# Optimization experiments

Measured on AMD Instinct MI355X. Metric: run time of the kernel, lower is better.

Reference implementation:

```python
import jax, jax.numpy as jnp
import numpy as np

B, S, I, H, A = 512, 256, 12, 256, 9


def _lstm_layer(x, w_ih, w_hh, b_ih, b_hh):
    # x: [B,S,in] -> outputs [B,S,H], final (h, c). PyTorch gate order i,f,g,o.
    b, s, _ = x.shape
    h_dim = w_hh.shape[1]
    xg = jnp.einsum('bsi,gi->bsg', x, w_ih) + b_ih  # [B,S,4H] precomputed input gates

    def step(carry, xg_t):
        h, c = carry
        gates = xg_t + h @ w_hh.T + b_hh
        i_g, f_g, g_g, o_g = jnp.split(gates, 4, axis=-1)
        c = jax.nn.sigmoid(f_g) * c + jax.nn.sigmoid(i_g) * jnp.tanh(g_g)
        h = jax.nn.sigmoid(o_g) * jnp.tanh(c)
        return (h, c), h

    init = (jnp.zeros((b, h_dim), x.dtype), jnp.zeros((b, h_dim), x.dtype))
    (h, c), ys = jax.lax.scan(step, init, jnp.swapaxes(xg, 0, 1))
    return jnp.swapaxes(ys, 0, 1), h, c


def setup_inputs() -> dict:
    key = jax.random.key(0)
    ks = jax.random.split(key, 20)
    sc = 0.1
    inp = {
        'x': jax.random.normal(ks[0], (B, S, I), jnp.float32),
        'mask': jnp.ones((B, A), jnp.float32),
        'W_emb': jax.random.normal(ks[1], (H, I), jnp.float32) * sc,
        'b_emb': jnp.zeros((H,), jnp.float32),
        'w_ih0': jax.random.normal(ks[2], (4 * H, H), jnp.float32) * sc,
        'w_hh0': jax.random.normal(ks[3], (4 * H, H), jnp.float32) * sc,
        'b_ih0': jnp.zeros((4 * H,), jnp.float32),
        'b_hh0': jnp.zeros((4 * H,), jnp.float32),
        'w_ih1': jax.random.normal(ks[4], (4 * H, H), jnp.float32) * sc,
        'w_hh1': jax.random.normal(ks[5], (4 * H, H), jnp.float32) * sc,
        'b_ih1': jnp.zeros((4 * H,), jnp.float32),
        'b_hh1': jnp.zeros((4 * H,), jnp.float32),
        'ln_g': jnp.ones((H,), jnp.float32),
        'ln_b': jnp.zeros((H,), jnp.float32),
        'w1': jax.random.normal(ks[6], (32, H), jnp.float32) * sc,
        'b1': jnp.zeros((32,), jnp.float32),
        'w2': jax.random.normal(ks[7], (A, 32), jnp.float32) * sc,
        'b2': jnp.zeros((A,), jnp.float32),
    }
    return inp


def reference(x, mask, W_emb, b_emb, w_ih0, w_hh0, b_ih0, b_hh0,
              w_ih1, w_hh1, b_ih1, b_hh1, ln_g, ln_b, w1, b1, w2, b2):
    # embed + ReLU
    emb = jax.nn.relu(jnp.einsum('bsi,hi->bsh', x, W_emb) + b_emb)  # [B,S,H]
    # 2-layer LSTM (dropout between layers is identity in eval mode)
    y0, h0, c0 = _lstm_layer(emb, w_ih0, w_hh0, b_ih0, b_hh0)
    y1, h1, c1 = _lstm_layer(y0, w_ih1, w_hh1, b_ih1, b_hh1)
    last = y1[:, -1, :]  # [B,H]
    # LayerNorm
    mu = jnp.mean(last, axis=-1, keepdims=True)
    var = jnp.mean((last - mu) ** 2, axis=-1, keepdims=True)
    normed = (last - mu) / jnp.sqrt(var + 1e-5) * ln_g + ln_b
    # MLP head (dropout identity in eval)
    hdn = jax.nn.relu(normed @ w1.T + b1)
    logits = hdn @ w2.T + b2  # [B,A]
    logits = logits + (1.0 - mask) * -1e9
    hidden = (jnp.stack([h0, h1]), jnp.stack([c0, c1]))
    return logits, hidden
```

## Files before the change

kernel.cpp:

```cpp
#include <hip/hip_runtime.h>
#include <cstdint>
#include <cstddef>

typedef __attribute__((ext_vector_type(8))) short short8;
typedef __attribute__((ext_vector_type(4))) float f32x4;

#define MFMA16(a, b, c) __builtin_amdgcn_mfma_f32_16x16x32_bf16((a), (b), (c), 0, 0, 0)

constexpr int kB = 512, kS = 256, kI = 12, kH = 256, kA = 9;
constexpr int kNS = 8;
constexpr int kNB = 32;
constexpr int kT  = 512;
constexpr int LDH = 264;
constexpr int LDG = 132;
constexpr int kBH = kB * kH;
constexpr int FLS = kS * kNS;

constexpr int OUT_H = kB * kA;
constexpr int OUT_C = OUT_H + 2 * kBH;

__device__ __forceinline__ short f2bf(float f) {
  uint32_t u = __float_as_uint(f);
  u += 0x7fffu + ((u >> 16) & 1u);
  return (short)(u >> 16);
}
__device__ __forceinline__ float fast_sigmoid(float v) {
  return __builtin_amdgcn_rcpf(1.f + __expf(-v));
}
__device__ __forceinline__ float fast_tanh(float v) {
  return 2.f * __builtin_amdgcn_rcpf(1.f + __expf(-2.f * v)) - 1.f;
}

__global__ __launch_bounds__(kT) void lstm_scan_kernel(
    const float* __restrict__ x,
    const float* __restrict__ W_emb, const float* __restrict__ b_emb,
    const float* __restrict__ w_ih0, const float* __restrict__ w_hh0,
    const float* __restrict__ b_ih0, const float* __restrict__ b_hh0,
    const float* __restrict__ w_ih1, const float* __restrict__ w_hh1,
    const float* __restrict__ b_ih1, const float* __restrict__ b_hh1,
    unsigned short* __restrict__ h0ex, unsigned short* __restrict__ h1ex,
    int* __restrict__ flags,
    float* __restrict__ dout)
{
  const int tid   = threadIdx.x;
  const int btile = blockIdx.x & (kNB - 1);
  const int slice = blockIdx.x >> 5;
  const int b0    = btile * 16;
  const int lane  = tid & 63;
  const int wave  = tid >> 6;
  const int n16   = lane & 15;
  const int quad  = lane >> 4;

  __shared__ short embL[2][16 * LDH];
  __shared__ short hA[16 * LDH];
  __shared__ short hB[16 * LDH];
  __shared__ float gL0[16 * LDG];
  __shared__ float gL1[16 * LDG];

  for (int i = tid; i < 16 * LDH; i += kT) { hA[i] = 0; hB[i] = 0; }

  const float* Wm[4] = { w_ih0, w_hh0, w_ih1, w_hh1 };
  short8 wB[4][8];
  {
    const int gcol = (wave >> 1) * kH + slice * 32 + (wave & 1) * 16 + n16;
#pragma unroll
    for (int mat = 0; mat < 4; ++mat) {
      const float* wp = Wm[mat] + (size_t)gcol * kH;
#pragma unroll
      for (int kk = 0; kk < 8; ++kk) {
        const float* p = wp + kk * 32 + quad * 8;
        const float4 f0 = *(const float4*)p;
        const float4 f1 = *(const float4*)(p + 4);
        short8 v;
        v[0] = f2bf(f0.x); v[1] = f2bf(f0.y); v[2] = f2bf(f0.z); v[3] = f2bf(f0.w);
        v[4] = f2bf(f1.x); v[5] = f2bf(f1.y); v[6] = f2bf(f1.z); v[7] = f2bf(f1.w);
        wB[mat][kk] = v;
      }
    }
  }
  short8 wE[2];
  float bembv[2];
#pragma unroll
  for (int i = 0; i < 2; ++i) {
    const int col = wave * 32 + i * 16 + n16;
    short8 v;
#pragma unroll
    for (int j = 0; j < 8; ++j) {
      const int k = quad * 8 + j;
      v[j] = (k < kI) ? f2bf(W_emb[col * kI + k]) : (short)0;
    }
    wE[i] = v;
    bembv[i] = b_emb[col];
  }
  const int erow = tid >> 5;
  const int ec   = tid & 31;
  const int ecol = slice * 32 + ec;
  float bi0[4], bi1[4];
#pragma unroll
  for (int g = 0; g < 4; ++g) {
    bi0[g] = b_ih0[g * kH + ecol] + b_hh0[g * kH + ecol];
    bi1[g] = b_ih1[g * kH + ecol] + b_hh1[g * kH + ecol];
  }
  float c0v = 0.f, c1v = 0.f;

#define EMB_TILE(DST, T)                                                    \
  {                                                                         \
    const float* xr = x + ((size_t)(b0 + n16) * kS + (T)) * kI;             \
    short8 xa;                                                              \
    _Pragma("unroll")                                                       \
    for (int j = 0; j < 8; ++j) {                                           \
      const int k = quad * 8 + j;                                           \
      xa[j] = (k < kI) ? f2bf(xr[k]) : (short)0;                            \
    }                                                                       \
    _Pragma("unroll")                                                       \
    for (int i = 0; i < 2; ++i) {                                           \
      f32x4 zz = {0.f, 0.f, 0.f, 0.f};                                      \
      f32x4 e = MFMA16(xa, wE[i], zz);                                      \
      const int col = wave * 32 + i * 16 + n16;                             \
      _Pragma("unroll")                                                     \
      for (int r = 0; r < 4; ++r) {                                         \
        float v = e[r] + bembv[i];                                          \
        v = v > 0.f ? v : 0.f;                                              \
        (DST)[(quad * 4 + r) * LDH + col] = f2bf(v);                        \
      }                                                                     \
    }                                                                       \
  }

  EMB_TILE(embL[0], 0);
  EMB_TILE(embL[1], 1);
  __syncthreads();
  f32x4 zcur = {0.f, 0.f, 0.f, 0.f};
#pragma unroll
  for (int kk = 0; kk < 8; ++kk) {
    const short8 e = *(const short8*)&embL[0][n16 * LDH + kk * 32 + quad * 8];
    zcur = MFMA16(e, wB[0][kk], zcur);
  }

  int* const fl = flags + btile * FLS;

  for (int p = 0; p <= kS; ++p) {
    const int par = p & 1;

    {
      f32x4 a0 = zcur;
      f32x4 g1 = {0.f, 0.f, 0.f, 0.f};
#pragma unroll
      for (int kk = 0; kk < 8; ++kk) {
        const short8 ha = *(const short8*)&hA[n16 * LDH + kk * 32 + quad * 8];
        a0 = MFMA16(ha, wB[1][kk], a0);
        g1 = MFMA16(ha, wB[2][kk], g1);
      }
#pragma unroll
      for (int kk = 0; kk < 8; ++kk) {
        const short8 hb = *(const short8*)&hB[n16 * LDH + kk * 32 + quad * 8];
        g1 = MFMA16(hb, wB[3][kk], g1);
      }
      const int lcol = (wave >> 1) * 32 + (wave & 1) * 16 + n16;
#pragma unroll
      for (int r = 0; r < 4; ++r) {
        gL0[(quad * 4 + r) * LDG + lcol] = a0[r];
        gL1[(quad * 4 + r) * LDG + lcol] = g1[r];
      }
    }
    __syncthreads();

    if (p < kS) {
      const float iv = gL0[erow * LDG +       ec] + bi0[0];
      const float fv = gL0[erow * LDG +  32 + ec] + bi0[1];
      const float gv = gL0[erow * LDG +  64 + ec] + bi0[2];
      const float ov = gL0[erow * LDG +  96 + ec] + bi0[3];
      const float c = fast_sigmoid(fv) * c0v + fast_sigmoid(iv) * fast_tanh(gv);
      c0v = c;
      const float h = fast_sigmoid(ov) * fast_tanh(c);
      unsigned short* dst = &h0ex[(size_t)par * kBH + (size_t)(b0 + erow) * kH + ecol];
      __hip_atomic_store(dst, (unsigned short)f2bf(h), __ATOMIC_RELAXED, __HIP_MEMORY_SCOPE_AGENT);
      if (p == kS - 1) {
        dout[OUT_H + (size_t)(b0 + erow) * kH + ecol] = h;
        dout[OUT_C + (size_t)(b0 + erow) * kH + ecol] = c;
      }
    }
    if (p >= 1) {
      const float iv = gL1[erow * LDG +       ec] + bi1[0];
      const float fv = gL1[erow * LDG +  32 + ec] + bi1[1];
      const float gv = gL1[erow * LDG +  64 + ec] + bi1[2];
      const float ov = gL1[erow * LDG +  96 + ec] + bi1[3];
      const float c = fast_sigmoid(fv) * c1v + fast_sigmoid(iv) * fast_tanh(gv);
      c1v = c;
      const float h = fast_sigmoid(ov) * fast_tanh(c);
      unsigned short* dst = &h1ex[(size_t)par * kBH + (size_t)(b0 + erow) * kH + ecol];
      __hip_atomic_store(dst, (unsigned short)f2bf(h), __ATOMIC_RELAXED, __HIP_MEMORY_SCOPE_AGENT);
      if (p == kS) {
        dout[OUT_H + kBH + (size_t)(b0 + erow) * kH + ecol] = h;
        dout[OUT_C + kBH + (size_t)(b0 + erow) * kH + ecol] = c;
      }
    }
    __syncthreads();

    if (p < kS) {
      if (tid == 0)
        __hip_atomic_store(fl + p * kNS + slice, p + 1,
                           __ATOMIC_RELAXED, __HIP_MEMORY_SCOPE_AGENT);

      f32x4 z = {0.f, 0.f, 0.f, 0.f};
#pragma unroll
      for (int kk = 0; kk < 8; ++kk) {
        const short8 e = *(const short8*)&embL[par ^ 1][n16 * LDH + kk * 32 + quad * 8];
        z = MFMA16(e, wB[0][kk], z);
      }

      {
        const uint64_t* f64 = (const uint64_t*)(fl + p * kNS);
        const int tgt = p + 1;
        for (;;) {
          uint64_t v0 = __hip_atomic_load(f64 + 0, __ATOMIC_RELAXED, __HIP_MEMORY_SCOPE_AGENT);
          uint64_t v1 = __hip_atomic_load(f64 + 1, __ATOMIC_RELAXED, __HIP_MEMORY_SCOPE_AGENT);
          uint64_t v2 = __hip_atomic_load(f64 + 2, __ATOMIC_RELAXED, __HIP_MEMORY_SCOPE_AGENT);
          uint64_t v3 = __hip_atomic_load(f64 + 3, __ATOMIC_RELAXED, __HIP_MEMORY_SCOPE_AGENT);
          if ((int)(v0 & 0xffffffffu) >= tgt && (int)(v0 >> 32) >= tgt &&
              (int)(v1 & 0xffffffffu) >= tgt && (int)(v1 >> 32) >= tgt &&
              (int)(v2 & 0xffffffffu) >= tgt && (int)(v2 >> 32) >= tgt &&
              (int)(v3 & 0xffffffffu) >= tgt && (int)(v3 >> 32) >= tgt)
            break;
          __builtin_amdgcn_s_sleep(1);
        }
      }

      const int rr = tid >> 5;
      const int cc = (tid & 31) * 8;
      const size_t base = (size_t)par * kBH + (size_t)(b0 + rr) * kH + cc;
      const uint64_t* s0 = (const uint64_t*)&h0ex[base];
      const uint64_t* s1 = (const uint64_t*)&h1ex[base];
      uint64_t va0 = __hip_atomic_load(s0 + 0, __ATOMIC_RELAXED, __HIP_MEMORY_SCOPE_AGENT);
      uint64_t va1 = __hip_atomic_load(s0 + 1, __ATOMIC_RELAXED, __HIP_MEMORY_SCOPE_AGENT);
      uint64_t vb0 = __hip_atomic_load(s1 + 0, __ATOMIC_RELAXED, __HIP_MEMORY_SCOPE_AGENT);
      uint64_t vb1 = __hip_atomic_load(s1 + 1, __ATOMIC_RELAXED, __HIP_MEMORY_SCOPE_AGENT);

      if (p + 2 < kS) EMB_TILE(embL[par], p + 2);

      uint64_t* dA = (uint64_t*)&hA[rr * LDH + cc];
      uint64_t* dB = (uint64_t*)&hB[rr * LDH + cc];
      dA[0] = va0; dA[1] = va1;
      dB[0] = vb0; dB[1] = vb1;
      __syncthreads();
      zcur = z;
    }
  }
#undef EMB_TILE
}

__global__ __launch_bounds__(64) void head_kernel(
    const float* __restrict__ h1last, const float* __restrict__ mask,
    const float* __restrict__ ln_g, const float* __restrict__ ln_b,
    const float* __restrict__ w1, const float* __restrict__ b1,
    const float* __restrict__ w2, const float* __restrict__ b2,
    float* __restrict__ out)
{
  const int r = blockIdx.x;
  const int lane = threadIdx.x;
  __shared__ float ns[kH];
  __shared__ float hd[32];
  const float4 v = *(const float4*)&h1last[r * kH + lane * 4];
  float vv[4] = {v.x, v.y, v.z, v.w};
  float s = vv[0] + vv[1] + vv[2] + vv[3];
#pragma unroll
  for (int off = 32; off > 0; off >>= 1) s += __shfl_xor(s, off, 64);
  const float mean = s * (1.f / kH);
  float q = 0.f;
#pragma unroll
  for (int j = 0; j < 4; ++j) { const float d = vv[j] - mean; q += d * d; }
#pragma unroll
  for (int off = 32; off > 0; off >>= 1) q += __shfl_xor(q, off, 64);
  const float rstd = rsqrtf(q * (1.f / kH) + 1e-5f);
#pragma unroll
  for (int j = 0; j < 4; ++j) {
    const int c = lane * 4 + j;
    ns[c] = (vv[j] - mean) * rstd * ln_g[c] + ln_b[c];
  }
  __syncthreads();
  if (lane < 32) {
    float a = b1[lane];
    const float* wr = w1 + lane * kH;
    for (int k = 0; k < kH; ++k) a += ns[k] * wr[k];
    hd[lane] = a > 0.f ? a : 0.f;
  }
  __syncthreads();
  if (lane < kA) {
    float a = b2[lane];
    const float* wr = w2 + lane * 32;
#pragma unroll
    for (int k = 0; k < 32; ++k) a += hd[k] * wr[k];
    a += (1.f - mask[r * kA + lane]) * (-1e9f);
    out[r * kA + lane] = a;
  }
}

extern "C" void kernel_launch(void* const* d_in, const int* in_sizes, int n_in,
                              void* d_out, int out_size, void* d_ws, size_t ws_size,
                              hipStream_t stream)
{
  (void)in_sizes; (void)n_in; (void)out_size; (void)ws_size;
  const float* x     = (const float*)d_in[0];
  const float* mask  = (const float*)d_in[1];
  const float* W_emb = (const float*)d_in[2];
  const float* b_emb = (const float*)d_in[3];
  const float* w_ih0 = (const float*)d_in[4];
  const float* w_hh0 = (const float*)d_in[5];
  const float* b_ih0 = (const float*)d_in[6];
  const float* b_hh0 = (const float*)d_in[7];
  const float* w_ih1 = (const float*)d_in[8];
  const float* w_hh1 = (const float*)d_in[9];
  const float* b_ih1 = (const float*)d_in[10];
  const float* b_hh1 = (const float*)d_in[11];
  const float* ln_g  = (const float*)d_in[12];
  const float* ln_b  = (const float*)d_in[13];
  const float* w1    = (const float*)d_in[14];
  const float* b1    = (const float*)d_in[15];
  const float* w2    = (const float*)d_in[16];
  const float* b2    = (const float*)d_in[17];
  float* out = (float*)d_out;

  unsigned short* h0ex = (unsigned short*)d_ws;
  unsigned short* h1ex = h0ex + 2 * kBH;
  int* flags = (int*)(h1ex + 2 * kBH);
  const size_t flag_bytes = (size_t)kNB * FLS * sizeof(int);

  hipMemsetAsync(flags, 0, flag_bytes, stream);
  hipMemsetAsync(h1ex, 0, (size_t)kBH * sizeof(unsigned short), stream);

  lstm_scan_kernel<<<dim3(kNB * kNS), dim3(kT), 0, stream>>>(
      x, W_emb, b_emb, w_ih0, w_hh0, b_ih0, b_hh0, w_ih1, w_hh1, b_ih1, b_hh1,
      h0ex, h1ex, flags, out);

  head_kernel<<<dim3(kB), dim3(64), 0, stream>>>(
      out + OUT_H + kBH, mask, ln_g, ln_b, w1, b1, w2, b2, out);
}
```

Before: 1.018 ms.

## Split hidden columns across 16 slices with 256-thread blocks, two per CU

Each batch tile's hidden dimension is now split into 16 slices instead of 8, giving 512 blocks of 256 threads with launch bounds allowing two blocks per CU. The block-to-tile mapping is swizzled so the two halves interleave. Each block now handles 16 gate columns, so per-step work per block is halved, but every block waits on 16 flags instead of 8. The input-gate product for layer 0 is no longer precomputed ahead of time; it is computed inside the step alongside the recurrent product, and the embedding uses a single buffer filled one step ahead. This adds more cross-block synchronisation and puts the embedding work back on the critical path, in exchange for more parallelism per step.

```diff
diff --git a/kernel.cpp b/kernel.cpp
--- a/kernel.cpp
+++ b/kernel.cpp
@@ -8,11 +8,11 @@
 #define MFMA16(a, b, c) __builtin_amdgcn_mfma_f32_16x16x32_bf16((a), (b), (c), 0, 0, 0)
 
 constexpr int kB = 512, kS = 256, kI = 12, kH = 256, kA = 9;
-constexpr int kNS = 8;
+constexpr int kNS = 16;
 constexpr int kNB = 32;
-constexpr int kT  = 512;
+constexpr int kT  = 256;
 constexpr int LDH = 264;
-constexpr int LDG = 132;
+constexpr int LDG2 = 68;
 constexpr int kBH = kB * kH;
 constexpr int FLS = kS * kNS;
 
@@ -31,7 +31,7 @@
   return 2.f * __builtin_amdgcn_rcpf(1.f + __expf(-2.f * v)) - 1.f;
 }
 
-__global__ __launch_bounds__(kT) void lstm_scan_kernel(
+__global__ __launch_bounds__(kT, 2) void lstm_scan_kernel(
     const float* __restrict__ x,
     const float* __restrict__ W_emb, const float* __restrict__ b_emb,
     const float* __restrict__ w_ih0, const float* __restrict__ w_hh0,
@@ -42,27 +42,30 @@
     int* __restrict__ flags,
     float* __restrict__ dout)
 {
-  const int tid   = threadIdx.x;
-  const int btile = blockIdx.x & (kNB - 1);
-  const int slice = blockIdx.x >> 5;
+  const int tid  = threadIdx.x;
+  const int bid  = blockIdx.x;
+  const int half = bid >> 8;
+  const int b8   = bid & 255;
+  const int btile = (b8 & 31) ^ (half << 4);
+  const int slice = (b8 >> 5) + half * 8;
   const int b0    = btile * 16;
   const int lane  = tid & 63;
   const int wave  = tid >> 6;
   const int n16   = lane & 15;
   const int quad  = lane >> 4;
 
-  __shared__ short embL[2][16 * LDH];
+  __shared__ short embL[16 * LDH];
   __shared__ short hA[16 * LDH];
   __shared__ short hB[16 * LDH];
-  __shared__ float gL0[16 * LDG];
-  __shared__ float gL1[16 * LDG];
+  __shared__ float gL0[16 * LDG2];
+  __shared__ float gL1[16 * LDG2];
 
   for (int i = tid; i < 16 * LDH; i += kT) { hA[i] = 0; hB[i] = 0; }
 
   const float* Wm[4] = { w_ih0, w_hh0, w_ih1, w_hh1 };
   short8 wB[4][8];
   {
-    const int gcol = (wave >> 1) * kH + slice * 32 + (wave & 1) * 16 + n16;
+    const int gcol = wave * kH + slice * 16 + n16;
 #pragma unroll
     for (int mat = 0; mat < 4; ++mat) {
       const float* wp = Wm[mat] + (size_t)gcol * kH;
@@ -78,11 +81,11 @@
       }
     }
   }
-  short8 wE[2];
-  float bembv[2];
-#pragma unroll
-  for (int i = 0; i < 2; ++i) {
-    const int col = wave * 32 + i * 16 + n16;
+  short8 wE[4];
+  float bembv[4];
+#pragma unroll
+  for (int i = 0; i < 4; ++i) {
+    const int col = wave * 64 + i * 16 + n16;
     short8 v;
 #pragma unroll
     for (int j = 0; j < 8; ++j) {
@@ -92,9 +95,9 @@
     wE[i] = v;
     bembv[i] = b_emb[col];
   }
-  const int erow = tid >> 5;
-  const int ec   = tid & 31;
-  const int ecol = slice * 32 + ec;
+  const int erow = tid >> 4;
+  const int ec   = tid & 15;
+  const int ecol = slice * 16 + ec;
   float bi0[4], bi1[4];
 #pragma unroll
   for (int g = 0; g < 4; ++g) {
@@ -103,7 +106,7 @@
   }
   float c0v = 0.f, c1v = 0.f;
 
-#define EMB_TILE(DST, T)                                                    \
+#define EMB_TILE(T)                                                         \
   {                                                                         \
     const float* xr = x + ((size_t)(b0 + n16) * kS + (T)) * kI;             \
     short8 xa;                                                              \
@@ -113,28 +116,21 @@
       xa[j] = (k < kI) ? f2bf(xr[k]) : (short)0;                            \
     }                                                                       \
     _Pragma("unroll")                                                       \
-    for (int i = 0; i < 2; ++i) {                                           \
+    for (int i = 0; i < 4; ++i) {                                           \
       f32x4 zz = {0.f, 0.f, 0.f, 0.f};                                      \
       f32x4 e = MFMA16(xa, wE[i], zz);                                      \
-      const int col = wave * 32 + i * 16 + n16;                             \
+      const int col = wave * 64 + i * 16 + n16;                             \
       _Pragma("unroll")                                                     \
       for (int r = 0; r < 4; ++r) {                                         \
         float v = e[r] + bembv[i];                                          \
         v = v > 0.f ? v : 0.f;                                              \
-        (DST)[(quad * 4 + r) * LDH + col] = f2bf(v);                        \
+        embL[(quad * 4 + r) * LDH + col] = f2bf(v);                         \
       }                                                                     \
     }                                                                       \
   }
 
-  EMB_TILE(embL[0], 0);
-  EMB_TILE(embL[1], 1);
+  EMB_TILE(0);
   __syncthreads();
-  f32x4 zcur = {0.f, 0.f, 0.f, 0.f};
-#pragma unroll
-  for (int kk = 0; kk < 8; ++kk) {
-    const short8 e = *(const short8*)&embL[0][n16 * LDH + kk * 32 + quad * 8];
-    zcur = MFMA16(e, wB[0][kk], zcur);
-  }
 
   int* const fl = flags + btile * FLS;
 
@@ -142,8 +138,7 @@
     const int par = p & 1;
 
     {
-      f32x4 a0 = zcur;
-      f32x4 g1 = {0.f, 0.f, 0.f, 0.f};
+      f32x4 a0 = {0.f,0.f,0.f,0.f}, g1 = a0;
 #pragma unroll
       for (int kk = 0; kk < 8; ++kk) {
         const short8 ha = *(const short8*)&hA[n16 * LDH + kk * 32 + quad * 8];
@@ -152,23 +147,28 @@
       }
 #pragma unroll
       for (int kk = 0; kk < 8; ++kk) {
+        const short8 e = *(const short8*)&embL[n16 * LDH + kk * 32 + quad * 8];
+        a0 = MFMA16(e, wB[0][kk], a0);
+      }
+#pragma unroll
+      for (int kk = 0; kk < 8; ++kk) {
         const short8 hb = *(const short8*)&hB[n16 * LDH + kk * 32 + quad * 8];
         g1 = MFMA16(hb, wB[3][kk], g1);
       }
-      const int lcol = (wave >> 1) * 32 + (wave & 1) * 16 + n16;
+      const int lcol = wave * 16 + n16;
 #pragma unroll
       for (int r = 0; r < 4; ++r) {
-        gL0[(quad * 4 + r) * LDG + lcol] = a0[r];
-        gL1[(quad * 4 + r) * LDG + lcol] = g1[r];
+        gL0[(quad * 4 + r) * LDG2 + lcol] = a0[r];
+        gL1[(quad * 4 + r) * LDG2 + lcol] = g1[r];
       }
     }
     __syncthreads();
 
     if (p < kS) {
-      const float iv = gL0[erow * LDG +       ec] + bi0[0];
-      const float fv = gL0[erow * LDG +  32 + ec] + bi0[1];
-      const float gv = gL0[erow * LDG +  64 + ec] + bi0[2];
-      const float ov = gL0[erow * LDG +  96 + ec] + bi0[3];
+      const float iv = gL0[erow * LDG2 +      ec] + bi0[0];
+      const float fv = gL0[erow * LDG2 + 16 + ec] + bi0[1];
+      const float gv = gL0[erow * LDG2 + 32 + ec] + bi0[2];
+      const float ov = gL0[erow * LDG2 + 48 + ec] + bi0[3];
       const float c = fast_sigmoid(fv) * c0v + fast_sigmoid(iv) * fast_tanh(gv);
       c0v = c;
       const float h = fast_sigmoid(ov) * fast_tanh(c);
@@ -180,10 +180,10 @@
       }
     }
     if (p >= 1) {
-      const float iv = gL1[erow * LDG +       ec] + bi1[0];
-      const float fv = gL1[erow * LDG +  32 + ec] + bi1[1];
-      const float gv = gL1[erow * LDG +  64 + ec] + bi1[2];
-      const float ov = gL1[erow * LDG +  96 + ec] + bi1[3];
+      const float iv = gL1[erow * LDG2 +      ec] + bi1[0];
+      const float fv = gL1[erow * LDG2 + 16 + ec] + bi1[1];
+      const float gv = gL1[erow * LDG2 + 32 + ec] + bi1[2];
+      const float ov = gL1[erow * LDG2 + 48 + ec] + bi1[3];
       const float c = fast_sigmoid(fv) * c1v + fast_sigmoid(iv) * fast_tanh(gv);
       c1v = c;
       const float h = fast_sigmoid(ov) * fast_tanh(c);
@@ -201,12 +201,7 @@
         __hip_atomic_store(fl + p * kNS + slice, p + 1,
                            __ATOMIC_RELAXED, __HIP_MEMORY_SCOPE_AGENT);
 
-      f32x4 z = {0.f, 0.f, 0.f, 0.f};
-#pragma unroll
-      for (int kk = 0; kk < 8; ++kk) {
-        const short8 e = *(const short8*)&embL[par ^ 1][n16 * LDH + kk * 32 + quad * 8];
-        z = MFMA16(e, wB[0][kk], z);
-      }
+      if (p + 1 < kS) EMB_TILE(p + 1);
 
       {
         const uint64_t* f64 = (const uint64_t*)(fl + p * kNS);
@@ -216,33 +211,43 @@
           uint64_t v1 = __hip_atomic_load(f64 + 1, __ATOMIC_RELAXED, __HIP_MEMORY_SCOPE_AGENT);
           uint64_t v2 = __hip_atomic_load(f64 + 2, __ATOMIC_RELAXED, __HIP_MEMORY_SCOPE_AGENT);
           uint64_t v3 = __hip_atomic_load(f64 + 3, __ATOMIC_RELAXED, __HIP_MEMORY_SCOPE_AGENT);
+          uint64_t v4 = __hip_atomic_load(f64 + 4, __ATOMIC_RELAXED, __HIP_MEMORY_SCOPE_AGENT);
+          uint64_t v5 = __hip_atomic_load(f64 + 5, __ATOMIC_RELAXED, __HIP_MEMORY_SCOPE_AGENT);
+          uint64_t v6 = __hip_atomic_load(f64 + 6, __ATOMIC_RELAXED, __HIP_MEMORY_SCOPE_AGENT);
+          uint64_t v7 = __hip_atomic_load(f64 + 7, __ATOMIC_RELAXED, __HIP_MEMORY_SCOPE_AGENT);
           if ((int)(v0 & 0xffffffffu) >= tgt && (int)(v0 >> 32) >= tgt &&
               (int)(v1 & 0xffffffffu) >= tgt && (int)(v1 >> 32) >= tgt &&
               (int)(v2 & 0xffffffffu) >= tgt && (int)(v2 >> 32) >= tgt &&
-              (int)(v3 & 0xffffffffu) >= tgt && (int)(v3 >> 32) >= tgt)
+              (int)(v3 & 0xffffffffu) >= tgt && (int)(v3 >> 32) >= tgt &&
+              (int)(v4 & 0xffffffffu) >= tgt && (int)(v4 >> 32) >= tgt &&
+              (int)(v5 & 0xffffffffu) >= tgt && (int)(v5 >> 32) >= tgt &&
+              (int)(v6 & 0xffffffffu) >= tgt && (int)(v6 >> 32) >= tgt &&
+              (int)(v7 & 0xffffffffu) >= tgt && (int)(v7 >> 32) >= tgt)
             break;
           __builtin_amdgcn_s_sleep(1);
         }
       }
 
-      const int rr = tid >> 5;
-      const int cc = (tid & 31) * 8;
-      const size_t base = (size_t)par * kBH + (size_t)(b0 + rr) * kH + cc;
-      const uint64_t* s0 = (const uint64_t*)&h0ex[base];
-      const uint64_t* s1 = (const uint64_t*)&h1ex[base];
-      uint64_t va0 = __hip_atomic_load(s0 + 0, __ATOMIC_RELAXED, __HIP_MEMORY_SCOPE_AGENT);
-      uint64_t va1 = __hip_atomic_load(s0 + 1, __ATOMIC_RELAXED, __HIP_MEMORY_SCOPE_AGENT);
-      uint64_t vb0 = __hip_atomic_load(s1 + 0, __ATOMIC_RELAXED, __HIP_MEMORY_SCOPE_AGENT);
-      uint64_t vb1 = __hip_atomic_load(s1 + 1, __ATOMIC_RELAXED, __HIP_MEMORY_SCOPE_AGENT);
-
-      if (p + 2 < kS) EMB_TILE(embL[par], p + 2);
-
-      uint64_t* dA = (uint64_t*)&hA[rr * LDH + cc];
-      uint64_t* dB = (uint64_t*)&hB[rr * LDH + cc];
-      dA[0] = va0; dA[1] = va1;
-      dB[0] = vb0; dB[1] = vb1;
+      {
+        const int rr = tid >> 4;
+        const int cc = (tid & 15) * 16;
+        const size_t base = (size_t)par * kBH + (size_t)(b0 + rr) * kH + cc;
+        const uint64_t* s0 = (const uint64_t*)&h0ex[base];
+        const uint64_t* s1 = (const uint64_t*)&h1ex[base];
+        uint64_t a0 = __hip_atomic_load(s0 + 0, __ATOMIC_RELAXED, __HIP_MEMORY_SCOPE_AGENT);
+        uint64_t a1 = __hip_atomic_load(s0 + 1, __ATOMIC_RELAXED, __HIP_MEMORY_SCOPE_AGENT);
+        uint64_t a2 = __hip_atomic_load(s0 + 2, __ATOMIC_RELAXED, __HIP_MEMORY_SCOPE_AGENT);
+        uint64_t a3 = __hip_atomic_load(s0 + 3, __ATOMIC_RELAXED, __HIP_MEMORY_SCOPE_AGENT);
+        uint64_t b0_ = __hip_atomic_load(s1 + 0, __ATOMIC_RELAXED, __HIP_MEMORY_SCOPE_AGENT);
+        uint64_t b1_ = __hip_atomic_load(s1 + 1, __ATOMIC_RELAXED, __HIP_MEMORY_SCOPE_AGENT);
+        uint64_t b2_ = __hip_atomic_load(s1 + 2, __ATOMIC_RELAXED, __HIP_MEMORY_SCOPE_AGENT);
+        uint64_t b3_ = __hip_atomic_load(s1 + 3, __ATOMIC_RELAXED, __HIP_MEMORY_SCOPE_AGENT);
+        uint64_t* dA = (uint64_t*)&hA[rr * LDH + cc];
+        uint64_t* dB = (uint64_t*)&hB[rr * LDH + cc];
+        dA[0] = a0; dA[1] = a1; dA[2] = a2; dA[3] = a3;
+        dB[0] = b0_; dB[1] = b1_; dB[2] = b2_; dB[3] = b3_;
+      }
       __syncthreads();
-      zcur = z;
     }
   }
 #undef EMB_TILE
```

Result: slower. 1.450 ms (+42.4%).

## Specialize waves into producer/consumer roles with in-register gate math and byte flags

Applied to the files above, without the earlier changes.

Waves are split by role. Some compute the input projection (embedding→z) or the layer-1 input projection and write partial gates to LDS. Others compute the recurrent h·W_hh product and apply the LSTM cell directly on the MFMA accumulators in registers. This removes the separate gate-scatter/gather phase and one block-wide barrier per step. Cross-block synchronisation moves from per-slice int counters to per-wave byte flags, so readiness is checked with four 64-bit loads, and the h buffers in LDS become double-buffered. The cost is uneven per-wave work, and only four waves poll and copy the exchanged hidden state.

```diff
diff --git a/kernel.cpp b/kernel.cpp
--- a/kernel.cpp
+++ b/kernel.cpp
@@ -12,9 +12,7 @@
 constexpr int kNB = 32;
 constexpr int kT  = 512;
 constexpr int LDH = 264;
-constexpr int LDG = 132;
 constexpr int kBH = kB * kH;
-constexpr int FLS = kS * kNS;
 
 constexpr int OUT_H = kB * kA;
 constexpr int OUT_C = OUT_H + 2 * kBH;
@@ -39,7 +37,7 @@
     const float* __restrict__ w_ih1, const float* __restrict__ w_hh1,
     const float* __restrict__ b_ih1, const float* __restrict__ b_hh1,
     unsigned short* __restrict__ h0ex, unsigned short* __restrict__ h1ex,
-    int* __restrict__ flags,
+    unsigned char* __restrict__ flags,
     float* __restrict__ dout)
 {
   const int tid   = threadIdx.x;
@@ -50,60 +48,65 @@
   const int wave  = tid >> 6;
   const int n16   = lane & 15;
   const int quad  = lane >> 4;
+  const int L     = wave >> 2;
+  const int U     = (wave >> 1) & 1;
+  const int R     = wave & 1;
 
   __shared__ short embL[2][16 * LDH];
-  __shared__ short hA[16 * LDH];
-  __shared__ short hB[16 * LDH];
-  __shared__ float gL0[16 * LDG];
-  __shared__ float gL1[16 * LDG];
-
-  for (int i = tid; i < 16 * LDH; i += kT) { hA[i] = 0; hB[i] = 0; }
-
-  const float* Wm[4] = { w_ih0, w_hh0, w_ih1, w_hh1 };
+  __shared__ short hAb[2][16 * LDH];
+  __shared__ short hBb[2][16 * LDH];
+  __shared__ float gZ[2 * 2 * 4 * 256];
+  __shared__ float gP[2 * 4 * 256];
+
+  for (int i = tid; i < 16 * LDH; i += kT) { hAb[0][i] = 0; hBb[0][i] = 0; }
+
+  const float* mat = (L == 0) ? (R == 0 ? w_ih0 : w_hh0)
+                              : (R == 0 ? w_hh1 : w_ih1);
   short8 wB[4][8];
   {
-    const int gcol = (wave >> 1) * kH + slice * 32 + (wave & 1) * 16 + n16;
-#pragma unroll
-    for (int mat = 0; mat < 4; ++mat) {
-      const float* wp = Wm[mat] + (size_t)gcol * kH;
+#pragma unroll
+    for (int t = 0; t < 4; ++t) {
+      const int gcol = t * kH + slice * 32 + U * 16 + n16;
+      const float* wp = mat + (size_t)gcol * kH;
 #pragma unroll
       for (int kk = 0; kk < 8; ++kk) {
-        const float* p = wp + kk * 32 + quad * 8;
-        const float4 f0 = *(const float4*)p;
-        const float4 f1 = *(const float4*)(p + 4);
+        const float* p4 = wp + kk * 32 + quad * 8;
+        const float4 f0 = *(const float4*)p4;
+        const float4 f1 = *(const float4*)(p4 + 4);
         short8 v;
         v[0] = f2bf(f0.x); v[1] = f2bf(f0.y); v[2] = f2bf(f0.z); v[3] = f2bf(f0.w);
         v[4] = f2bf(f1.x); v[5] = f2bf(f1.y); v[6] = f2bf(f1.z); v[7] = f2bf(f1.w);
-        wB[mat][kk] = v;
-      }
-    }
-  }
-  short8 wE[2];
-  float bembv[2];
-#pragma unroll
-  for (int i = 0; i < 2; ++i) {
-    const int col = wave * 32 + i * 16 + n16;
-    short8 v;
-#pragma unroll
-    for (int j = 0; j < 8; ++j) {
-      const int k = quad * 8 + j;
-      v[j] = (k < kI) ? f2bf(W_emb[col * kI + k]) : (short)0;
-    }
-    wE[i] = v;
-    bembv[i] = b_emb[col];
-  }
-  const int erow = tid >> 5;
-  const int ec   = tid & 31;
-  const int ecol = slice * 32 + ec;
-  float bi0[4], bi1[4];
-#pragma unroll
-  for (int g = 0; g < 4; ++g) {
-    bi0[g] = b_ih0[g * kH + ecol] + b_hh0[g * kH + ecol];
-    bi1[g] = b_ih1[g * kH + ecol] + b_hh1[g * kH + ecol];
-  }
-  float c0v = 0.f, c1v = 0.f;
-
-#define EMB_TILE(DST, T)                                                    \
+        wB[t][kk] = v;
+      }
+    }
+  }
+  short8 wE[8];
+  float bembv[8];
+  if (L == 0 && R == 0) {
+#pragma unroll
+    for (int i = 0; i < 8; ++i) {
+      const int col = U * 128 + i * 16 + n16;
+      short8 v;
+#pragma unroll
+      for (int j = 0; j < 8; ++j) {
+        const int k = quad * 8 + j;
+        v[j] = (k < kI) ? f2bf(W_emb[col * kI + k]) : (short)0;
+      }
+      wE[i] = v;
+      bembv[i] = b_emb[col];
+    }
+  }
+  const int ecol = slice * 32 + U * 16 + n16;
+  float bi[4] = {0.f, 0.f, 0.f, 0.f};
+  if (R == 1) {
+    const float* bih = L ? b_ih1 : b_ih0;
+    const float* bhh = L ? b_hh1 : b_hh0;
+#pragma unroll
+    for (int t = 0; t < 4; ++t) bi[t] = bih[t * kH + ecol] + bhh[t * kH + ecol];
+  }
+  f32x4 cst = {0.f, 0.f, 0.f, 0.f};
+
+#define EMB8(BUF, T)                                                        \
   {                                                                         \
     const float* xr = x + ((size_t)(b0 + n16) * kS + (T)) * kI;             \
     short8 xa;                                                              \
@@ -113,139 +116,167 @@
       xa[j] = (k < kI) ? f2bf(xr[k]) : (short)0;                            \
     }                                                                       \
     _Pragma("unroll")                                                       \
-    for (int i = 0; i < 2; ++i) {                                           \
+    for (int i = 0; i < 8; ++i) {                                           \
       f32x4 zz = {0.f, 0.f, 0.f, 0.f};                                      \
       f32x4 e = MFMA16(xa, wE[i], zz);                                      \
-      const int col = wave * 32 + i * 16 + n16;                             \
+      const int col = U * 128 + i * 16 + n16;                               \
       _Pragma("unroll")                                                     \
       for (int r = 0; r < 4; ++r) {                                         \
         float v = e[r] + bembv[i];                                          \
         v = v > 0.f ? v : 0.f;                                              \
-        (DST)[(quad * 4 + r) * LDH + col] = f2bf(v);                        \
+        (BUF)[(quad * 4 + r) * LDH + col] = f2bf(v);                        \
       }                                                                     \
     }                                                                       \
   }
 
-  EMB_TILE(embL[0], 0);
-  EMB_TILE(embL[1], 1);
+  if (L == 0 && R == 0) { EMB8(embL[0], 0) EMB8(embL[1], 1) }
   __syncthreads();
-  f32x4 zcur = {0.f, 0.f, 0.f, 0.f};
-#pragma unroll
-  for (int kk = 0; kk < 8; ++kk) {
-    const short8 e = *(const short8*)&embL[0][n16 * LDH + kk * 32 + quad * 8];
-    zcur = MFMA16(e, wB[0][kk], zcur);
-  }
-
-  int* const fl = flags + btile * FLS;
+  if (L == 0 && R == 0) {
+    f32x4 a0 = {0.f,0.f,0.f,0.f}, a1 = a0, a2 = a0, a3 = a0;
+#pragma unroll
+    for (int kk = 0; kk < 8; ++kk) {
+      const short8 e = *(const short8*)&embL[0][n16 * LDH + kk * 32 + quad * 8];
+      a0 = MFMA16(e, wB[0][kk], a0);
+      a1 = MFMA16(e, wB[1][kk], a1);
+      a2 = MFMA16(e, wB[2][kk], a2);
+      a3 = MFMA16(e, wB[3][kk], a3);
+    }
+    const int gzb = (U * 4) * 256 + lane * 4;
+    *(f32x4*)&gZ[gzb +   0] = a0;
+    *(f32x4*)&gZ[gzb + 256] = a1;
+    *(f32x4*)&gZ[gzb + 512] = a2;
+    *(f32x4*)&gZ[gzb + 768] = a3;
+  }
+
+  unsigned char* const flB = flags + (size_t)btile * kS * 32;
+  const uint64_t kOnes = 0x0101010101010101ULL;
 
   for (int p = 0; p <= kS; ++p) {
     const int par = p & 1;
-
-    {
-      f32x4 a0 = zcur;
-      f32x4 g1 = {0.f, 0.f, 0.f, 0.f};
-#pragma unroll
-      for (int kk = 0; kk < 8; ++kk) {
-        const short8 ha = *(const short8*)&hA[n16 * LDH + kk * 32 + quad * 8];
-        a0 = MFMA16(ha, wB[1][kk], a0);
-        g1 = MFMA16(ha, wB[2][kk], g1);
-      }
-#pragma unroll
-      for (int kk = 0; kk < 8; ++kk) {
-        const short8 hb = *(const short8*)&hB[n16 * LDH + kk * 32 + quad * 8];
-        g1 = MFMA16(hb, wB[3][kk], g1);
-      }
-      const int lcol = (wave >> 1) * 32 + (wave & 1) * 16 + n16;
-#pragma unroll
-      for (int r = 0; r < 4; ++r) {
-        gL0[(quad * 4 + r) * LDG + lcol] = a0[r];
-        gL1[(quad * 4 + r) * LDG + lcol] = g1[r];
+    f32x4 acc0 = {0.f,0.f,0.f,0.f}, acc1 = acc0, acc2 = acc0, acc3 = acc0;
+
+    if (R == 0) {
+      if (L == 1) {
+        const short* hb = hBb[par];
+#pragma unroll
+        for (int kk = 0; kk < 8; ++kk) {
+          const short8 e = *(const short8*)&hb[n16 * LDH + kk * 32 + quad * 8];
+          acc0 = MFMA16(e, wB[0][kk], acc0);
+          acc1 = MFMA16(e, wB[1][kk], acc1);
+          acc2 = MFMA16(e, wB[2][kk], acc2);
+          acc3 = MFMA16(e, wB[3][kk], acc3);
+        }
+        const int gpb = (U * 4) * 256 + lane * 4;
+        *(f32x4*)&gP[gpb +   0] = acc0;
+        *(f32x4*)&gP[gpb + 256] = acc1;
+        *(f32x4*)&gP[gpb + 512] = acc2;
+        *(f32x4*)&gP[gpb + 768] = acc3;
+      } else {
+        if (p + 1 < kS) {
+          const short* eb = embL[par ^ 1];
+#pragma unroll
+          for (int kk = 0; kk < 8; ++kk) {
+            const short8 e = *(const short8*)&eb[n16 * LDH + kk * 32 + quad * 8];
+            acc0 = MFMA16(e, wB[0][kk], acc0);
+            acc1 = MFMA16(e, wB[1][kk], acc1);
+            acc2 = MFMA16(e, wB[2][kk], acc2);
+            acc3 = MFMA16(e, wB[3][kk], acc3);
+          }
+          const int gzb = (((par ^ 1) * 2 + U) * 4) * 256 + lane * 4;
+          *(f32x4*)&gZ[gzb +   0] = acc0;
+          *(f32x4*)&gZ[gzb + 256] = acc1;
+          *(f32x4*)&gZ[gzb + 512] = acc2;
+          *(f32x4*)&gZ[gzb + 768] = acc3;
+        }
+        if (p + 2 < kS) { EMB8(embL[par], p + 2) }
+      }
+    } else {
+      const bool act = (L == 0) ? (p < kS) : (p >= 1);
+      if (act) {
+        const short* ha = hAb[par];
+#pragma unroll
+        for (int kk = 0; kk < 8; ++kk) {
+          const short8 e = *(const short8*)&ha[n16 * LDH + kk * 32 + quad * 8];
+          acc0 = MFMA16(e, wB[0][kk], acc0);
+          acc1 = MFMA16(e, wB[1][kk], acc1);
+          acc2 = MFMA16(e, wB[2][kk], acc2);
+          acc3 = MFMA16(e, wB[3][kk], acc3);
+        }
       }
     }
     __syncthreads();
 
-    if (p < kS) {
-      const float iv = gL0[erow * LDG +       ec] + bi0[0];
-      const float fv = gL0[erow * LDG +  32 + ec] + bi0[1];
-      const float gv = gL0[erow * LDG +  64 + ec] + bi0[2];
-      const float ov = gL0[erow * LDG +  96 + ec] + bi0[3];
-      const float c = fast_sigmoid(fv) * c0v + fast_sigmoid(iv) * fast_tanh(gv);
-      c0v = c;
-      const float h = fast_sigmoid(ov) * fast_tanh(c);
-      unsigned short* dst = &h0ex[(size_t)par * kBH + (size_t)(b0 + erow) * kH + ecol];
-      __hip_atomic_store(dst, (unsigned short)f2bf(h), __ATOMIC_RELAXED, __HIP_MEMORY_SCOPE_AGENT);
-      if (p == kS - 1) {
-        dout[OUT_H + (size_t)(b0 + erow) * kH + ecol] = h;
-        dout[OUT_C + (size_t)(b0 + erow) * kH + ecol] = c;
-      }
-    }
-    if (p >= 1) {
-      const float iv = gL1[erow * LDG +       ec] + bi1[0];
-      const float fv = gL1[erow * LDG +  32 + ec] + bi1[1];
-      const float gv = gL1[erow * LDG +  64 + ec] + bi1[2];
-      const float ov = gL1[erow * LDG +  96 + ec] + bi1[3];
-      const float c = fast_sigmoid(fv) * c1v + fast_sigmoid(iv) * fast_tanh(gv);
-      c1v = c;
-      const float h = fast_sigmoid(ov) * fast_tanh(c);
-      unsigned short* dst = &h1ex[(size_t)par * kBH + (size_t)(b0 + erow) * kH + ecol];
-      __hip_atomic_store(dst, (unsigned short)f2bf(h), __ATOMIC_RELAXED, __HIP_MEMORY_SCOPE_AGENT);
-      if (p == kS) {
-        dout[OUT_H + kBH + (size_t)(b0 + erow) * kH + ecol] = h;
-        dout[OUT_C + kBH + (size_t)(b0 + erow) * kH + ecol] = c;
-      }
-    }
-    __syncthreads();
-
-    if (p < kS) {
-      if (tid == 0)
-        __hip_atomic_store(fl + p * kNS + slice, p + 1,
-                           __ATOMIC_RELAXED, __HIP_MEMORY_SCOPE_AGENT);
-
-      f32x4 z = {0.f, 0.f, 0.f, 0.f};
-#pragma unroll
-      for (int kk = 0; kk < 8; ++kk) {
-        const short8 e = *(const short8*)&embL[par ^ 1][n16 * LDH + kk * 32 + quad * 8];
-        z = MFMA16(e, wB[0][kk], z);
-      }
-
-      {
-        const uint64_t* f64 = (const uint64_t*)(fl + p * kNS);
-        const int tgt = p + 1;
-        for (;;) {
-          uint64_t v0 = __hip_atomic_load(f64 + 0, __ATOMIC_RELAXED, __HIP_MEMORY_SCOPE_AGENT);
-          uint64_t v1 = __hip_atomic_load(f64 + 1, __ATOMIC_RELAXED, __HIP_MEMORY_SCOPE_AGENT);
-          uint64_t v2 = __hip_atomic_load(f64 + 2, __ATOMIC_RELAXED, __HIP_MEMORY_SCOPE_AGENT);
-          uint64_t v3 = __hip_atomic_load(f64 + 3, __ATOMIC_RELAXED, __HIP_MEMORY_SCOPE_AGENT);
-          if ((int)(v0 & 0xffffffffu) >= tgt && (int)(v0 >> 32) >= tgt &&
-              (int)(v1 & 0xffffffffu) >= tgt && (int)(v1 >> 32) >= tgt &&
-              (int)(v2 & 0xffffffffu) >= tgt && (int)(v2 >> 32) >= tgt &&
-              (int)(v3 & 0xffffffffu) >= tgt && (int)(v3 >> 32) >= tgt)
-            break;
-          __builtin_amdgcn_s_sleep(1);
+    if (R == 1) {
+      const bool act = (L == 0) ? (p < kS) : (p >= 1);
+      if (act) {
+        const float* part = (L == 0) ? &gZ[((par * 2 + U) * 4) * 256 + lane * 4]
+                                     : &gP[(U * 4) * 256 + lane * 4];
+        acc0 += *(const f32x4*)(part +   0);
+        acc1 += *(const f32x4*)(part + 256);
+        acc2 += *(const f32x4*)(part + 512);
+        acc3 += *(const f32x4*)(part + 768);
+        unsigned short* hex = (L == 0) ? h0ex : h1ex;
+        const size_t hbase = (size_t)par * kBH;
+#pragma unroll
+        for (int r = 0; r < 4; ++r) {
+          const float iv = acc0[r] + bi[0];
+          const float fv = acc1[r] + bi[1];
+          const float gv = acc2[r] + bi[2];
+          const float ov = acc3[r] + bi[3];
+          const float c = fast_sigmoid(fv) * cst[r] + fast_sigmoid(iv) * fast_tanh(gv);
+          cst[r] = c;
+          const float h = fast_sigmoid(ov) * fast_tanh(c);
+          const int row = b0 + quad * 4 + r;
+          __hip_atomic_store(&hex[hbase + (size_t)row * kH + ecol],
+                             (unsigned short)f2bf(h),
+                             __ATOMIC_RELAXED, __HIP_MEMORY_SCOPE_AGENT);
+          if ((L == 0 && p == kS - 1) || (L == 1 && p == kS)) {
+            dout[OUT_H + (size_t)L * kBH + (size_t)row * kH + ecol] = h;
+            dout[OUT_C + (size_t)L * kBH + (size_t)row * kH + ecol] = c;
+          }
         }
       }
-
-      const int rr = tid >> 5;
-      const int cc = (tid & 31) * 8;
+      if (p < kS) {
+        asm volatile("s_waitcnt vmcnt(0)" ::: "memory");
+        if (lane == 0)
+          __hip_atomic_store(flB + (size_t)p * 32 + slice * 4 + L * 2 + U,
+                             (unsigned char)1,
+                             __ATOMIC_RELAXED, __HIP_MEMORY_SCOPE_AGENT);
+      }
+    } else if (p < kS) {
+      const uint64_t* f64 = (const uint64_t*)(flB + (size_t)p * 32);
+      int spins = 0;
+      for (;;) {
+        const uint64_t v0 = __hip_atomic_load(f64 + 0, __ATOMIC_RELAXED, __HIP_MEMORY_SCOPE_AGENT);
+        const uint64_t v1 = __hip_atomic_load(f64 + 1, __ATOMIC_RELAXED, __HIP_MEMORY_SCOPE_AGENT);
+        const uint64_t v2 = __hip_atomic_load(f64 + 2, __ATOMIC_RELAXED, __HIP_MEMORY_SCOPE_AGENT);
+        const uint64_t v3 = __hip_atomic_load(f64 + 3, __ATOMIC_RELAXED, __HIP_MEMORY_SCOPE_AGENT);
+        if (v0 == kOnes && v1 == kOnes && v2 == kOnes && v3 == kOnes) break;
+        if (++spins > 256) __builtin_amdgcn_s_sleep(8);
+        else               __builtin_amdgcn_s_sleep(1);
+      }
+      const int rtid = (wave >> 1) * 64 + lane;
+      const int rr = rtid >> 4;
+      const int cc = (rtid & 15) * 16;
       const size_t base = (size_t)par * kBH + (size_t)(b0 + rr) * kH + cc;
       const uint64_t* s0 = (const uint64_t*)&h0ex[base];
       const uint64_t* s1 = (const uint64_t*)&h1ex[base];
-      uint64_t va0 = __hip_atomic_load(s0 + 0, __ATOMIC_RELAXED, __HIP_MEMORY_SCOPE_AGENT);
-      uint64_t va1 = __hip_atomic_load(s0 + 1, __ATOMIC_RELAXED, __HIP_MEMORY_SCOPE_AGENT);
-      uint64_t vb0 = __hip_atomic_load(s1 + 0, __ATOMIC_RELAXED, __HIP_MEMORY_SCOPE_AGENT);
-      uint64_t vb1 = __hip_atomic_load(s1 + 1, __ATOMIC_RELAXED, __HIP_MEMORY_SCOPE_AGENT);
-
-      if (p + 2 < kS) EMB_TILE(embL[par], p + 2);
-
-      uint64_t* dA = (uint64_t*)&hA[rr * LDH + cc];
-      uint64_t* dB = (uint64_t*)&hB[rr * LDH + cc];
-      dA[0] = va0; dA[1] = va1;
-      dB[0] = vb0; dB[1] = vb1;
-      __syncthreads();
-      zcur = z;
-    }
-  }
-#undef EMB_TILE
+      const uint64_t ga0 = __hip_atomic_load(s0 + 0, __ATOMIC_RELAXED, __HIP_MEMORY_SCOPE_AGENT);
+      const uint64_t ga1 = __hip_atomic_load(s0 + 1, __ATOMIC_RELAXED, __HIP_MEMORY_SCOPE_AGENT);
+      const uint64_t ga2 = __hip_atomic_load(s0 + 2, __ATOMIC_RELAXED, __HIP_MEMORY_SCOPE_AGENT);
+      const uint64_t ga3 = __hip_atomic_load(s0 + 3, __ATOMIC_RELAXED, __HIP_MEMORY_SCOPE_AGENT);
+      const uint64_t gb0 = __hip_atomic_load(s1 + 0, __ATOMIC_RELAXED, __HIP_MEMORY_SCOPE_AGENT);
+      const uint64_t gb1 = __hip_atomic_load(s1 + 1, __ATOMIC_RELAXED, __HIP_MEMORY_SCOPE_AGENT);
+      const uint64_t gb2 = __hip_atomic_load(s1 + 2, __ATOMIC_RELAXED, __HIP_MEMORY_SCOPE_AGENT);
+      const uint64_t gb3 = __hip_atomic_load(s1 + 3, __ATOMIC_RELAXED, __HIP_MEMORY_SCOPE_AGENT);
+      uint64_t* dA = (uint64_t*)&hAb[par ^ 1][rr * LDH + cc];
+      uint64_t* dB = (uint64_t*)&hBb[par ^ 1][rr * LDH + cc];
+      dA[0] = ga0; dA[1] = ga1; dA[2] = ga2; dA[3] = ga3;
+      dB[0] = gb0; dB[1] = gb1; dB[2] = gb2; dB[3] = gb3;
+    }
+    __syncthreads();
+  }
+#undef EMB8
 }
 
 __global__ __launch_bounds__(64) void head_kernel(
@@ -321,8 +352,8 @@
 
   unsigned short* h0ex = (unsigned short*)d_ws;
   unsigned short* h1ex = h0ex + 2 * kBH;
-  int* flags = (int*)(h1ex + 2 * kBH);
-  const size_t flag_bytes = (size_t)kNB * FLS * sizeof(int);
+  unsigned char* flags = (unsigned char*)(h1ex + 2 * kBH);
+  const size_t flag_bytes = (size_t)kNB * kS * 32;
 
   hipMemsetAsync(flags, 0, flag_bytes, stream);
   hipMemsetAsync(h1ex, 0, (size_t)kBH * sizeof(unsigned short), stream);
```

Result: slower. 1.933 ms (+89.8%).
